# Optimization experiments

Hardware: AMD Instinct MI355X
Metric: run time of the kernel (lower is better)

## Reference

```python
import jax, jax.numpy as jnp
import numpy as np

N = 262144
C = 4096  # number of clusters


def _segment_max(x, seg, num_segments):
    # global_max_pool: per-cluster max over points
    return jax.ops.segment_max(x, seg, num_segments=num_segments)


def setup_inputs() -> dict:
    key = jax.random.key(0)
    ks = jax.random.split(key, 16)

    def lin(k, fan_in, fan_out):
        bound = 1.0 / np.sqrt(fan_in)
        kw, kb = jax.random.split(k)
        W = jax.random.uniform(kw, (fan_in, fan_out), jnp.float32, -bound, bound)
        b = jax.random.uniform(kb, (fan_out,), jnp.float32, -bound, bound)
        return W, b

    relative_points = jax.random.normal(ks[0], (N, 3), jnp.float32)
    features = jax.random.normal(ks[1], (N, 64), jnp.float32)
    cluster = jax.random.randint(ks[2], (N,), 0, C, jnp.int64)

    enc_W1, enc_b1 = lin(ks[3], 3, 32)    # neighborhood encoder MLP
    enc_W2, enc_b2 = lin(ks[4], 32, 64)
    W1, b1 = lin(ks[5], 3 + 64 + 64, 128)  # fc_layers (input_size + enc_out + 3)
    W2, b2 = lin(ks[6], 128, 128)
    G1, gb1 = lin(ks[7], 128, 128)          # fc_layers_global
    G2, gb2 = lin(ks[8], 128, 256)

    return dict(relative_points=relative_points, features=features, cluster=cluster,
                enc_W1=enc_W1, enc_b1=enc_b1, enc_W2=enc_W2, enc_b2=enc_b2,
                W1=W1, b1=b1, W2=W2, b2=b2, G1=G1, gb1=gb1, G2=G2, gb2=gb2)


def reference(relative_points, features, cluster,
              enc_W1, enc_b1, enc_W2, enc_b2,
              W1, b1, W2, b2, G1, gb1, G2, gb2):
    # --- neighborhood encoder: per-point MLP then per-cluster max-pool ---
    h = jax.nn.relu(relative_points @ enc_W1 + enc_b1)          # [N, 32]
    h = jax.nn.relu(h @ enc_W2 + enc_b2)                        # [N, 64]
    neigh_enc = _segment_max(h, cluster, C)                     # [C, 64]

    # gather-by-index duplication + concat
    dup = neigh_enc[cluster]                                    # [N, 64]
    encoded = jnp.concatenate([relative_points, features, dup], axis=1)  # [N, 131]

    # local fc stack (relu, leaky=False)
    encoded = jax.nn.relu(encoded @ W1 + b1)                    # [N, 128]
    encoded = jax.nn.relu(encoded @ W2 + b2)                    # [N, 128]

    # global_max_pool (mean=False)
    encoded_global = _segment_max(encoded, cluster, C)          # [C, 128]

    # global fc stack
    encoded_global = jax.nn.relu(encoded_global @ G1 + gb1)     # [C, 128]
    encoded_global = jax.nn.relu(encoded_global @ G2 + gb2)     # [C, 256]
    return encoded_global
```

## Files before the change

### kernel.cpp

```cpp
#include <hip/hip_runtime.h>
#include <hip/hip_bf16.h>

#define NN 262144
#define CC 4096
#define NBLK 64
#define PPB (NN / NBLK)
#define NT (NN / 64)
#define SLOTS 3

typedef __attribute__((ext_vector_type(8))) short bf16x8;
typedef __attribute__((ext_vector_type(4))) float f32x4;

__device__ __forceinline__ unsigned pk2(float a, float b) {
  __hip_bfloat16 ha = __float2bfloat16(a);
  __hip_bfloat16 hb = __float2bfloat16(b);
  unsigned short ua, ub;
  __builtin_memcpy(&ua, &ha, 2);
  __builtin_memcpy(&ub, &hb, 2);
  return (unsigned)ua | ((unsigned)ub << 16);
}

__global__ __launch_bounds__(256) void k_init(
    const int* __restrict__ cluster, unsigned* __restrict__ hist2d,
    const float* __restrict__ eW2, const float* __restrict__ W1,
    const float* __restrict__ W2, unsigned* __restrict__ packE,
    unsigned* __restrict__ pack1, unsigned* __restrict__ pack2)
{
  __shared__ unsigned h[CC];
  const int t = threadIdx.x, b = blockIdx.x;
  if (b < NBLK) {
    for (int q = t; q < CC; q += 256) h[q] = 0u;
    __syncthreads();
    const int base = b * PPB;
#pragma unroll 4
    for (int k = 0; k < PPB; k += 256) atomicAdd(&h[cluster[base + k + t]], 1u);
    __syncthreads();
    for (int q = t; q < CC; q += 256) hist2d[b * CC + q] = h[q];
    return;
  }
  const int id = (b - NBLK) * 256 + t;
  if (id < 1024) {
    const int nt = id >> 8, l = (id >> 2) & 63, v = id & 3;
    const int k0 = (l >> 4) * 8 + 2 * v, col = nt * 16 + (l & 15);
    packE[id] = pk2(eW2[k0 * 64 + col], eW2[(k0 + 1) * 64 + col]);
  } else if (id < 1024 + 6144) {
    const int j = id - 1024;
    const int kk = j >> 11, nt = (j >> 8) & 7, l = (j >> 2) & 63, v = j & 3;
    const int col = nt * 16 + (l & 15);
    float vals[2];
#pragma unroll
    for (int hh = 0; hh < 2; ++hh) {
      const int k = kk * 32 + (l >> 4) * 8 + 2 * v + hh;
      vals[hh] = (k < 64) ? W1[(3 + k) * 128 + col]
               : (k < 67) ? W1[(k - 64) * 128 + col] : 0.f;
    }
    pack1[j] = pk2(vals[0], vals[1]);
  } else {
    const int j = id - (1024 + 6144);
    const int kk = j >> 11, nt = (j >> 8) & 7, l = (j >> 2) & 63, v = j & 3;
    const int col = nt * 16 + (l & 15);
    const int k0 = kk * 32 + (l >> 4) * 4 + v;
    pack2[j] = pk2(W2[k0 * 128 + col], W2[(k0 + 16) * 128 + col]);
  }
}

#define ZERO_F4 589824
__global__ __launch_bounds__(256) void k_scan_a(
    const unsigned* __restrict__ hist2d, unsigned* __restrict__ base2d,
    unsigned* __restrict__ totals, float4* __restrict__ zbase)
{
  const int t = threadIdx.x, b = blockIdx.x;
  if (b < 16) {
    const int c = b * 256 + t;
    unsigned acc = 0;
#pragma unroll 4
    for (int bb = 0; bb < NBLK; ++bb) {
      const unsigned v = hist2d[bb * CC + c];
      base2d[bb * CC + c] = acc;
      acc += v;
    }
    totals[c] = acc;
  } else {
    const int zb = b - 16;
    const float4 z = {0.f, 0.f, 0.f, 0.f};
#pragma unroll 5
    for (int q = 0; q < 25; ++q) {
      const int idx = (zb * 25 + q) * 256 + t;
      if (idx < ZERO_F4) zbase[idx] = z;
    }
  }
}

__global__ __launch_bounds__(256) void k_scatter(
    const int* __restrict__ cluster, const unsigned* __restrict__ base2d,
    const unsigned* __restrict__ totals, unsigned* __restrict__ permcid,
    unsigned* __restrict__ cstart_g)
{
  __shared__ unsigned cur[CC];
  __shared__ unsigned part[256];
  const int t = threadIdx.x, b = blockIdx.x;
  unsigned loc[16];
  unsigned s = 0;
#pragma unroll
  for (int q = 0; q < 16; ++q) { loc[q] = s; s += totals[t * 16 + q]; }
  part[t] = s;
  __syncthreads();
  for (int off = 1; off < 256; off <<= 1) {
    const unsigned v = (t >= off) ? part[t - off] : 0u;
    __syncthreads();
    part[t] += v;
    __syncthreads();
  }
  const unsigned baset = part[t] - s;
#pragma unroll
  for (int q = 0; q < 16; ++q) {
    const unsigned cs = baset + loc[q];
    cur[t * 16 + q] = base2d[b * CC + t * 16 + q] + cs;
    if (b == 0) cstart_g[t * 16 + q] = cs;
  }
  __syncthreads();
  const int base = b * PPB;
#pragma unroll 4
  for (int k = 0; k < PPB; k += 256) {
    const int i = base + k + t;
    const int c = cluster[i];
    const unsigned pos = atomicAdd(&cur[c], 1u);
    permcid[pos] = (unsigned)i | ((unsigned)c << 18);
  }
}

__global__ __launch_bounds__(256) void k_enc_t(
    const float* __restrict__ pts, const unsigned* __restrict__ permcid,
    const unsigned* __restrict__ cstart,
    const float* __restrict__ eW1, const float* __restrict__ eb1,
    const float* __restrict__ eb2, const unsigned* __restrict__ packE,
    float* __restrict__ pse)
{
  __shared__ float P4[64 * 4];
  __shared__ unsigned h1s[64 * 20];
  __shared__ int seg_r0[65];
  __shared__ int seg_cid[64];
  __shared__ int seg_j[64];
  __shared__ int nseg_s;
  const int t = threadIdx.x;
  const int lane = t & 63, w = t >> 6;
  const int g = lane >> 4, ln15 = lane & 15;
  const int b = blockIdx.x;

  if (w == 0) {
    const unsigned pc = permcid[b * 64 + t];
    const int cid = (int)(pc >> 18);
    const int prevcid = (t == 0) ? -1 : (int)(permcid[b * 64 + t - 1] >> 18);
    const bool flag = (t == 0) || (prevcid != cid);
    const unsigned long long mask = __ballot(flag);
    const int rank = (int)__popcll(mask & ((1ull << t) - 1ull));
    if (flag) {
      seg_r0[rank] = t;
      seg_cid[rank] = cid;
      seg_j[rank] = b - (int)(cstart[cid] >> 6);
    }
    if (t == 0) {
      const int ns = (int)__popcll(mask);
      nseg_s = ns;
      seg_r0[ns] = 64;
    }
    const int i = (int)(pc & 0x3FFFFu);
    P4[t * 4 + 0] = pts[i * 3 + 0];
    P4[t * 4 + 1] = pts[i * 3 + 1];
    P4[t * 4 + 2] = pts[i * 3 + 2];
    P4[t * 4 + 3] = 0.f;
  }
  __syncthreads();
  {
    const int r = t >> 2, qq = t & 3;
    const float p0 = P4[r * 4], p1 = P4[r * 4 + 1], p2 = P4[r * 4 + 2];
    unsigned wv[4];
#pragma unroll
    for (int u = 0; u < 4; ++u) {
      float hv[2];
#pragma unroll
      for (int hh = 0; hh < 2; ++hh) {
        const int cc2 = qq * 8 + 2 * u + hh;
        hv[hh] = fmaxf(fmaf(p2, eW1[64 + cc2],
                       fmaf(p1, eW1[32 + cc2],
                       fmaf(p0, eW1[cc2], eb1[cc2]))), 0.f);
      }
      wv[u] = pk2(hv[0], hv[1]);
    }
    uint4 st; st.x = wv[0]; st.y = wv[1]; st.z = wv[2]; st.w = wv[3];
    *reinterpret_cast<uint4*>(&h1s[r * 20 + qq * 4]) = st;
  }
  __syncthreads();
  {
    const int col = w * 16 + ln15;
    const bf16x8 bfr = *reinterpret_cast<const bf16x8*>(&packE[(w * 64 + lane) * 4]);
    const float bias = eb2[col];
    f32x4 acc[4];
#pragma unroll
    for (int m = 0; m < 4; ++m) acc[m] = f32x4{bias, bias, bias, bias};
#pragma unroll
    for (int m = 0; m < 4; ++m) {
      const bf16x8 a = *reinterpret_cast<const bf16x8*>(&h1s[(16 * m + ln15) * 20 + g * 4]);
      acc[m] = __builtin_amdgcn_mfma_f32_16x16x32_bf16(a, bfr, acc[m], 0, 0, 0);
    }
    const int nseg = nseg_s;
    for (int s = 0; s < nseg; ++s) {
      const int r0 = seg_r0[s], r1 = seg_r0[s + 1];
      float v = 0.f;
#pragma unroll
      for (int m = 0; m < 4; ++m) {
        if (r0 < 16 * (m + 1) && r1 > 16 * m) {
#pragma unroll
          for (int q = 0; q < 4; ++q) {
            const int row = 16 * m + 4 * g + q;
            const bool in = (row >= r0) & (row < r1);
            v = fmaxf(v, in ? acc[m][q] : 0.f);
          }
        }
      }
      v = fmaxf(v, __shfl_xor(v, 16, 64));
      v = fmaxf(v, __shfl_xor(v, 32, 64));
      if (lane < 16) {
        const int c = seg_cid[s], j = seg_j[s];
        if (j < SLOTS - 1)
          pse[((size_t)c * SLOTS + j) * 64 + col] = v;
        else
          atomicMax((int*)&pse[((size_t)c * SLOTS + (SLOTS - 1)) * 64 + col],
                    __float_as_int(v));
      }
    }
  }
}

__global__ __launch_bounds__(256) void k_cproj2(
    const float* __restrict__ pse, const float* __restrict__ W1,
    const float* __restrict__ b1, float* __restrict__ cproj)
{
  __shared__ float nm2[2][64];
  const int t = threadIdx.x, b = blockIdx.x;
  if (t < 128) {
    const int rr = t >> 6, col = t & 63;
    const float* p = pse + ((size_t)(b * 2 + rr) * SLOTS) * 64 + col;
    nm2[rr][col] = fmaxf(fmaxf(p[0], p[64]), p[128]);
  }
  __syncthreads();
  const int rr = t >> 7, col = t & 127;
  const float* __restrict__ Wd = W1 + 67 * 128;
  float a = b1[col];
#pragma unroll 4
  for (int j = 0; j < 16; ++j) {
    const f32x4 nv = *reinterpret_cast<const f32x4*>(&nm2[rr][4 * j]);
    a = fmaf(nv[0], Wd[(4 * j + 0) * 128 + col], a);
    a = fmaf(nv[1], Wd[(4 * j + 1) * 128 + col], a);
    a = fmaf(nv[2], Wd[(4 * j + 2) * 128 + col], a);
    a = fmaf(nv[3], Wd[(4 * j + 3) * 128 + col], a);
  }
  cproj[(size_t)(b * 2 + rr) * 128 + col] = a;
}

__global__ __launch_bounds__(256) void k_fc_t(
    const float* __restrict__ pts, const float* __restrict__ feat,
    const unsigned* __restrict__ permcid, const unsigned* __restrict__ cstart,
    const float* __restrict__ b2, const float* __restrict__ cproj,
    const unsigned* __restrict__ pack1, const unsigned* __restrict__ pack2,
    float* __restrict__ psf)
{
  __shared__ unsigned buf[64 * 68];
  __shared__ float cpd[8][128];
  __shared__ int ridx_l[64];
  __shared__ int cid_l[64];
  __shared__ int seg_r0[65];
  __shared__ int seg_cid[64];
  __shared__ int seg_j[64];
  __shared__ int nseg_s;
  const int t = threadIdx.x;
  const int lane = t & 63, w = t >> 6;
  const int g = lane >> 4, ln15 = lane & 15;
  const int b = blockIdx.x;

  if (w == 0) {
    const unsigned pc = permcid[b * 64 + t];
    const int cid = (int)(pc >> 18);
    cid_l[t] = cid;
    const int prevcid = (t == 0) ? -1 : (int)(permcid[b * 64 + t - 1] >> 18);
    const bool flag = (t == 0) || (prevcid != cid);
    const unsigned long long mask = __ballot(flag);
    const int rank = (int)__popcll(mask & ((1ull << t) - 1ull));
    ridx_l[t] = (int)__popcll(mask & ((2ull << t) - 1ull)) - 1;
    if (flag) {
      seg_r0[rank] = t;
      seg_cid[rank] = cid;
      seg_j[rank] = b - (int)(cstart[cid] >> 6);
    }
    if (t == 0) {
      const int ns = (int)__popcll(mask);
      nseg_s = ns;
      seg_r0[ns] = 64;
    }
  }
  {
    const int r = t >> 2, seg = t & 3;
    const int i = (int)(permcid[b * 64 + r] & 0x3FFFFu);
    const float4* __restrict__ fp = reinterpret_cast<const float4*>(&feat[(size_t)i * 64 + seg * 16]);
    const float4 f0 = fp[0], f1 = fp[1], f2 = fp[2], f3 = fp[3];
    uint4 s0v, s1v;
    s0v.x = pk2(f0.x, f0.y); s0v.y = pk2(f0.z, f0.w);
    s0v.z = pk2(f1.x, f1.y); s0v.w = pk2(f1.z, f1.w);
    s1v.x = pk2(f2.x, f2.y); s1v.y = pk2(f2.z, f2.w);
    s1v.z = pk2(f3.x, f3.y); s1v.w = pk2(f3.z, f3.w);
    *reinterpret_cast<uint4*>(&buf[r * 52 + seg * 8 + 0]) = s0v;
    *reinterpret_cast<uint4*>(&buf[r * 52 + seg * 8 + 4]) = s1v;
  }
  if (t < 64) {
    const int i = (int)(permcid[b * 64 + t] & 0x3FFFFu);
    uint4 pw;
    pw.x = pk2(pts[i * 3 + 0], pts[i * 3 + 1]);
    pw.y = pk2(pts[i * 3 + 2], 0.f);
    pw.z = 0u; pw.w = 0u;
    uint4 zz; zz.x = zz.y = zz.z = zz.w = 0u;
    *reinterpret_cast<uint4*>(&buf[t * 52 + 32]) = pw;
    *reinterpret_cast<uint4*>(&buf[t * 52 + 36]) = zz;
    *reinterpret_cast<uint4*>(&buf[t * 52 + 40]) = zz;
    *reinterpret_cast<uint4*>(&buf[t * 52 + 44]) = zz;
  }
  __syncthreads();
  {
    const int nseg = nseg_s;
    const int lim = (nseg < 8) ? nseg : 8;
    for (int s = t >> 7; s < lim; s += 2)
      cpd[s][t & 127] = cproj[(size_t)seg_cid[s] * 128 + (t & 127)];
  }
  __syncthreads();

  const int colA = w * 32 + ln15, colB = colA + 16;
  f32x4 acc0[4], acc1[4];
  {
    const int nseg = nseg_s;
    if (nseg <= 2) {
      const float cA0 = cpd[0][colA], cA1 = cpd[0][colB];
      const float cB0 = (nseg == 2) ? cpd[1][colA] : cA0;
      const float cB1 = (nseg == 2) ? cpd[1][colB] : cA1;
      const int rb = (nseg == 2) ? seg_r0[1] : 64;
#pragma unroll
      for (int m = 0; m < 4; ++m)
#pragma unroll
        for (int q = 0; q < 4; ++q) {
          const int row = 16 * m + 4 * g + q;
          acc0[m][q] = (row < rb) ? cA0 : cB0;
          acc1[m][q] = (row < rb) ? cA1 : cB1;
        }
    } else {
#pragma unroll
      for (int m = 0; m < 4; ++m)
#pragma unroll
        for (int q = 0; q < 4; ++q) {
          const int row = 16 * m + 4 * g + q;
          const int idx = ridx_l[row];
          if (idx < 8) {
            acc0[m][q] = cpd[idx][colA];
            acc1[m][q] = cpd[idx][colB];
          } else {
            const int cc = cid_l[row];
            acc0[m][q] = cproj[(size_t)cc * 128 + colA];
            acc1[m][q] = cproj[(size_t)cc * 128 + colB];
          }
        }
    }
  }
  {
#pragma unroll
    for (int kk = 0; kk < 3; ++kk) {
      const bf16x8 bf0 = *reinterpret_cast<const bf16x8*>(&pack1[((kk * 8 + 2 * w + 0) * 64 + lane) * 4]);
      const bf16x8 bf1 = *reinterpret_cast<const bf16x8*>(&pack1[((kk * 8 + 2 * w + 1) * 64 + lane) * 4]);
#pragma unroll
      for (int m = 0; m < 4; ++m) {
        const bf16x8 a = *reinterpret_cast<const bf16x8*>(&buf[(16 * m + ln15) * 52 + kk * 16 + g * 4]);
        acc0[m] = __builtin_amdgcn_mfma_f32_16x16x32_bf16(a, bf0, acc0[m], 0, 0, 0);
        acc1[m] = __builtin_amdgcn_mfma_f32_16x16x32_bf16(a, bf1, acc1[m], 0, 0, 0);
      }
    }
  }
  __syncthreads();
  {
#pragma unroll
    for (int m = 0; m < 4; ++m)
#pragma unroll
      for (int q = 0; q < 4; ++q) {
        const int row = 16 * m + 4 * g + q;
        buf[row * 68 + w * 16 + ln15] =
            pk2(fmaxf(acc0[m][q], 0.f), fmaxf(acc1[m][q], 0.f));
      }
  }
  __syncthreads();
  {
    const float bb0 = b2[colA], bb1 = b2[colB];
#pragma unroll
    for (int m = 0; m < 4; ++m) {
      acc0[m] = f32x4{bb0, bb0, bb0, bb0};
      acc1[m] = f32x4{bb1, bb1, bb1, bb1};
    }
#pragma unroll
    for (int kk = 0; kk < 4; ++kk) {
      const bf16x8 bf0 = *reinterpret_cast<const bf16x8*>(&pack2[((kk * 8 + 2 * w + 0) * 64 + lane) * 4]);
      const bf16x8 bf1 = *reinterpret_cast<const bf16x8*>(&pack2[((kk * 8 + 2 * w + 1) * 64 + lane) * 4]);
#pragma unroll
      for (int m = 0; m < 4; ++m) {
        const bf16x8 a = *reinterpret_cast<const bf16x8*>(&buf[(16 * m + ln15) * 68 + kk * 16 + g * 4]);
        acc0[m] = __builtin_amdgcn_mfma_f32_16x16x32_bf16(a, bf0, acc0[m], 0, 0, 0);
        acc1[m] = __builtin_amdgcn_mfma_f32_16x16x32_bf16(a, bf1, acc1[m], 0, 0, 0);
      }
    }
  }
  {
    const int nseg = nseg_s;
    for (int s = 0; s < nseg; ++s) {
      const int r0 = seg_r0[s], r1 = seg_r0[s + 1];
      float v0 = 0.f, v1 = 0.f;
#pragma unroll
      for (int m = 0; m < 4; ++m) {
        if (r0 < 16 * (m + 1) && r1 > 16 * m) {
#pragma unroll
          for (int q = 0; q < 4; ++q) {
            const int row = 16 * m + 4 * g + q;
            const bool in = (row >= r0) & (row < r1);
            v0 = fmaxf(v0, in ? acc0[m][q] : 0.f);
            v1 = fmaxf(v1, in ? acc1[m][q] : 0.f);
          }
        }
      }
      v0 = fmaxf(v0, __shfl_xor(v0, 16, 64)); v0 = fmaxf(v0, __shfl_xor(v0, 32, 64));
      v1 = fmaxf(v1, __shfl_xor(v1, 16, 64)); v1 = fmaxf(v1, __shfl_xor(v1, 32, 64));
      if (lane < 16) {
        const int c = seg_cid[s], j = seg_j[s];
        if (j < SLOTS - 1) {
          psf[((size_t)c * SLOTS + j) * 128 + colA] = v0;
          psf[((size_t)c * SLOTS + j) * 128 + colB] = v1;
        } else {
          atomicMax((int*)&psf[((size_t)c * SLOTS + (SLOTS - 1)) * 128 + colA], __float_as_int(v0));
          atomicMax((int*)&psf[((size_t)c * SLOTS + (SLOTS - 1)) * 128 + colB], __float_as_int(v1));
        }
      }
    }
  }
}

__global__ __launch_bounds__(256) void k_glob(
    const float* __restrict__ psf, const float* __restrict__ G1,
    const float* __restrict__ gb1, const float* __restrict__ G2,
    const float* __restrict__ gb2, float* __restrict__ out)
{
  __shared__ float pooled[4][128];
  __shared__ float tg[4][128];
  const int t = threadIdx.x, b = blockIdx.x;
  const int c0 = b * 4;
#pragma unroll
  for (int q = 0; q < 2; ++q) {
    const int idx = q * 256 + t;
    const int cc = idx >> 7, col = idx & 127;
    const float* p = psf + (size_t)(c0 + cc) * (SLOTS * 128) + col;
    pooled[cc][col] = fmaxf(fmaxf(p[0], p[128]), p[256]);
  }
  __syncthreads();
  {
    const int col = t & 127, hi = t >> 7;
    float a0 = gb1[col], a1 = a0;
#pragma unroll 4
    for (int k = 0; k < 128; ++k) {
      const float wv = G1[k * 128 + col];
      a0 = fmaf(pooled[hi * 2 + 0][k], wv, a0);
      a1 = fmaf(pooled[hi * 2 + 1][k], wv, a1);
    }
    tg[hi * 2 + 0][col] = fmaxf(a0, 0.f);
    tg[hi * 2 + 1][col] = fmaxf(a1, 0.f);
  }
  __syncthreads();
  {
    float o[4];
#pragma unroll
    for (int q = 0; q < 4; ++q) o[q] = gb2[t];
#pragma unroll 2
    for (int k = 0; k < 128; ++k) {
      const float wv = G2[k * 256 + t];
#pragma unroll
      for (int q = 0; q < 4; ++q) o[q] = fmaf(tg[q][k], wv, o[q]);
    }
#pragma unroll
    for (int q = 0; q < 4; ++q)
      out[(size_t)(c0 + q) * 256 + t] = fmaxf(o[q], 0.f);
  }
}

extern "C" void kernel_launch(void* const* d_in, const int* in_sizes, int n_in,
                              void* d_out, int out_size, void* d_ws, size_t ws_size,
                              hipStream_t stream)
{
  (void)in_sizes; (void)n_in; (void)out_size; (void)ws_size;
  const float* pts  = (const float*)d_in[0];
  const float* feat = (const float*)d_in[1];
  const int*   clus = (const int*)  d_in[2];
  const float* eW1  = (const float*)d_in[3];
  const float* eb1  = (const float*)d_in[4];
  const float* eW2  = (const float*)d_in[5];
  const float* eb2  = (const float*)d_in[6];
  const float* W1   = (const float*)d_in[7];
  const float* b1   = (const float*)d_in[8];
  const float* W2   = (const float*)d_in[9];
  const float* b2   = (const float*)d_in[10];
  const float* G1   = (const float*)d_in[11];
  const float* gb1  = (const float*)d_in[12];
  const float* G2   = (const float*)d_in[13];
  const float* gb2  = (const float*)d_in[14];
  float* out = (float*)d_out;

  unsigned* ws      = (unsigned*)d_ws;
  unsigned* hist2d  = ws;
  unsigned* base2d  = ws + 262144;
  unsigned* totals  = ws + 524288;
  unsigned* cstart  = ws + 528384;
  unsigned* permcid = ws + 532480;
  unsigned* packE   = ws + 794624;
  unsigned* pack1   = ws + 795648;
  unsigned* pack2   = ws + 801792;
  float*    cproj   = (float*)(ws + 809984);
  float*    pse     = (float*)(ws + 1334272);
  float*    psf     = (float*)(ws + 2120704);

  k_init   <<<NBLK + 60, 256, 0, stream>>>(clus, hist2d, eW2, W1, W2,
                                           packE, pack1, pack2);
  k_scan_a <<<112, 256, 0, stream>>>(hist2d, base2d, totals, (float4*)pse);
  k_scatter<<<NBLK, 256, 0, stream>>>(clus, base2d, totals, permcid, cstart);
  k_enc_t  <<<NT, 256, 0, stream>>>(pts, permcid, cstart, eW1, eb1, eb2,
                                    packE, pse);
  k_cproj2 <<<CC / 2, 256, 0, stream>>>(pse, W1, b1, cproj);
  k_fc_t   <<<NT, 256, 0, stream>>>(pts, feat, permcid, cstart, b2, cproj,
                                    pack1, pack2, psf);
  k_glob   <<<1024, 256, 0, stream>>>(psf, G1, gb1, G2, gb2, out);
}
```

Before: 111.6 us.

## Double histogram blocks, move zeroing into scatter, simplify cproj bias add

```diff
diff --git a/kernel.cpp b/kernel.cpp
--- a/kernel.cpp
+++ b/kernel.cpp
@@ -3,7 +3,7 @@
 
 #define NN 262144
 #define CC 4096
-#define NBLK 64
+#define NBLK 128
 #define PPB (NN / NBLK)
 #define NT (NN / 64)
 #define SLOTS 3
@@ -64,41 +64,38 @@
   }
 }
 
-#define ZERO_F4 589824
 __global__ __launch_bounds__(256) void k_scan_a(
     const unsigned* __restrict__ hist2d, unsigned* __restrict__ base2d,
-    unsigned* __restrict__ totals, float4* __restrict__ zbase)
-{
-  const int t = threadIdx.x, b = blockIdx.x;
-  if (b < 16) {
-    const int c = b * 256 + t;
-    unsigned acc = 0;
+    unsigned* __restrict__ totals)
+{
+  const int c = blockIdx.x * 256 + threadIdx.x;
+  unsigned acc = 0;
 #pragma unroll 4
-    for (int bb = 0; bb < NBLK; ++bb) {
-      const unsigned v = hist2d[bb * CC + c];
-      base2d[bb * CC + c] = acc;
-      acc += v;
-    }
-    totals[c] = acc;
-  } else {
-    const int zb = b - 16;
-    const float4 z = {0.f, 0.f, 0.f, 0.f};
-#pragma unroll 5
-    for (int q = 0; q < 25; ++q) {
-      const int idx = (zb * 25 + q) * 256 + t;
-      if (idx < ZERO_F4) zbase[idx] = z;
-    }
-  }
-}
-
+  for (int bb = 0; bb < NBLK; ++bb) {
+    const unsigned v = hist2d[bb * CC + c];
+    base2d[bb * CC + c] = acc;
+    acc += v;
+  }
+  totals[c] = acc;
+}
+
+#define ZERO_F4 589824
 __global__ __launch_bounds__(256) void k_scatter(
     const int* __restrict__ cluster, const unsigned* __restrict__ base2d,
     const unsigned* __restrict__ totals, unsigned* __restrict__ permcid,
-    unsigned* __restrict__ cstart_g)
+    unsigned* __restrict__ cstart_g, float4* __restrict__ zbase)
 {
   __shared__ unsigned cur[CC];
   __shared__ unsigned part[256];
   const int t = threadIdx.x, b = blockIdx.x;
+  if (b >= NBLK) {
+    const int zb = b - NBLK;
+    const float4 z = {0.f, 0.f, 0.f, 0.f};
+#pragma unroll 4
+    for (int q = 0; q < 24; ++q)
+      zbase[(size_t)(zb * 24 + q) * 256 + t] = z;
+    return;
+  }
   unsigned loc[16];
   unsigned s = 0;
 #pragma unroll
@@ -266,8 +263,6 @@
     float* __restrict__ psf)
 {
   __shared__ unsigned buf[64 * 68];
-  __shared__ float cpd[8][128];
-  __shared__ int ridx_l[64];
   __shared__ int cid_l[64];
   __shared__ int seg_r0[65];
   __shared__ int seg_cid[64];
@@ -286,7 +281,6 @@
     const bool flag = (t == 0) || (prevcid != cid);
     const unsigned long long mask = __ballot(flag);
     const int rank = (int)__popcll(mask & ((1ull << t) - 1ull));
-    ridx_l[t] = (int)__popcll(mask & ((2ull << t) - 1ull)) - 1;
     if (flag) {
       seg_r0[rank] = t;
       seg_cid[rank] = cid;
@@ -324,50 +318,15 @@
     *reinterpret_cast<uint4*>(&buf[t * 52 + 44]) = zz;
   }
   __syncthreads();
-  {
-    const int nseg = nseg_s;
-    const int lim = (nseg < 8) ? nseg : 8;
-    for (int s = t >> 7; s < lim; s += 2)
-      cpd[s][t & 127] = cproj[(size_t)seg_cid[s] * 128 + (t & 127)];
-  }
-  __syncthreads();
 
   const int colA = w * 32 + ln15, colB = colA + 16;
   f32x4 acc0[4], acc1[4];
   {
-    const int nseg = nseg_s;
-    if (nseg <= 2) {
-      const float cA0 = cpd[0][colA], cA1 = cpd[0][colB];
-      const float cB0 = (nseg == 2) ? cpd[1][colA] : cA0;
-      const float cB1 = (nseg == 2) ? cpd[1][colB] : cA1;
-      const int rb = (nseg == 2) ? seg_r0[1] : 64;
-#pragma unroll
-      for (int m = 0; m < 4; ++m)
-#pragma unroll
-        for (int q = 0; q < 4; ++q) {
-          const int row = 16 * m + 4 * g + q;
-          acc0[m][q] = (row < rb) ? cA0 : cB0;
-          acc1[m][q] = (row < rb) ? cA1 : cB1;
-        }
-    } else {
-#pragma unroll
-      for (int m = 0; m < 4; ++m)
-#pragma unroll
-        for (int q = 0; q < 4; ++q) {
-          const int row = 16 * m + 4 * g + q;
-          const int idx = ridx_l[row];
-          if (idx < 8) {
-            acc0[m][q] = cpd[idx][colA];
-            acc1[m][q] = cpd[idx][colB];
-          } else {
-            const int cc = cid_l[row];
-            acc0[m][q] = cproj[(size_t)cc * 128 + colA];
-            acc1[m][q] = cproj[(size_t)cc * 128 + colB];
-          }
-        }
-    }
-  }
-  {
+#pragma unroll
+    for (int m = 0; m < 4; ++m) {
+      acc0[m] = f32x4{0.f, 0.f, 0.f, 0.f};
+      acc1[m] = f32x4{0.f, 0.f, 0.f, 0.f};
+    }
 #pragma unroll
     for (int kk = 0; kk < 3; ++kk) {
       const bf16x8 bf0 = *reinterpret_cast<const bf16x8*>(&pack1[((kk * 8 + 2 * w + 0) * 64 + lane) * 4]);
@@ -379,6 +338,15 @@
         acc1[m] = __builtin_amdgcn_mfma_f32_16x16x32_bf16(a, bf1, acc1[m], 0, 0, 0);
       }
     }
+#pragma unroll
+    for (int m = 0; m < 4; ++m)
+#pragma unroll
+      for (int q = 0; q < 4; ++q) {
+        const int row = 16 * m + 4 * g + q;
+        const int cc = cid_l[row];
+        acc0[m][q] += cproj[(size_t)cc * 128 + colA];
+        acc1[m][q] += cproj[(size_t)cc * 128 + colB];
+      }
   }
   __syncthreads();
   {
@@ -513,8 +481,7 @@
   float* out = (float*)d_out;
 
   unsigned* ws      = (unsigned*)d_ws;
-  unsigned* hist2d  = ws;
-  unsigned* base2d  = ws + 262144;
+  unsigned* base2d  = ws;
   unsigned* totals  = ws + 524288;
   unsigned* cstart  = ws + 528384;
   unsigned* permcid = ws + 532480;
@@ -524,11 +491,13 @@
   float*    cproj   = (float*)(ws + 809984);
   float*    pse     = (float*)(ws + 1334272);
   float*    psf     = (float*)(ws + 2120704);
+  unsigned* hist2d  = ws + 1334272;
 
   k_init   <<<NBLK + 60, 256, 0, stream>>>(clus, hist2d, eW2, W1, W2,
                                            packE, pack1, pack2);
-  k_scan_a <<<112, 256, 0, stream>>>(hist2d, base2d, totals, (float4*)pse);
-  k_scatter<<<NBLK, 256, 0, stream>>>(clus, base2d, totals, permcid, cstart);
+  k_scan_a <<<CC / 256, 256, 0, stream>>>(hist2d, base2d, totals);
+  k_scatter<<<NBLK + 96, 256, 0, stream>>>(clus, base2d, totals, permcid,
+                                           cstart, (float4*)pse);
   k_enc_t  <<<NT, 256, 0, stream>>>(pts, permcid, cstart, eW1, eb1, eb2,
                                     packE, pse);
   k_cproj2 <<<CC / 2, 256, 0, stream>>>(pse, W1, b1, cproj);
```

Measured after the change: 110.7 us. Within noise of the previous version (-0.8%).
